# Kernel optimization log

Hardware: AMD Instinct MI355X
Metric: run time of the kernel (lower is better)

The kernel has to match this reference:

```python
import jax, jax.numpy as jnp
import numpy as np

NE = 200000   # num_entities
NR = 16       # num_relations
D  = 128      # embed_dim
B  = 4096     # batch
S  = 64       # neighbors per node
L  = 2        # num_layers
H  = 4        # attention heads (hardcoded in module)


def _ln(x, g, b, eps=1e-5):
    m = jnp.mean(x, -1, keepdims=True)
    v = jnp.mean((x - m) ** 2, -1, keepdims=True)
    return (x - m) * jax.lax.rsqrt(v + eps) * g + b


def setup_inputs() -> dict:
    key = jax.random.key(0)
    ks = jax.random.split(key, 12)
    s = 0.05
    return {
        'drug_entity_indices': jax.random.randint(ks[0], (B,), 0, NE),
        'adj_entity': jax.random.randint(ks[1], (B, S), 0, NE),
        'adj_relation': jax.random.randint(ks[2], (B, S), 0, NR),
        'edge_weights': jax.random.uniform(ks[3], (B, S), dtype=jnp.float32),
        'entity_emb': jax.random.normal(ks[4], (NE, D), jnp.float32) * s,
        'W_rgcn': jax.random.normal(ks[5], (L, NR, D, D), jnp.float32) * s,
        'res_w': jax.random.normal(ks[6], (L, D, D), jnp.float32) * s,
        'res_b': jnp.zeros((L, D), jnp.float32),
        'proj_w': jax.random.normal(ks[7], (L, D, D), jnp.float32) * s,
        'proj_b': jnp.zeros((L, D), jnp.float32),
        'ln_g': jnp.ones((L, D), jnp.float32),
        'ln_b': jnp.zeros((L, D), jnp.float32),
        'in_proj_w': jax.random.normal(ks[8], (3 * D, D), jnp.float32) * s,
        'in_proj_b': jnp.zeros((3 * D,), jnp.float32),
        'out_proj_w': jax.random.normal(ks[9], (D, D), jnp.float32) * s,
        'out_proj_b': jnp.zeros((D,), jnp.float32),
        'fln_g': jnp.ones((D,), jnp.float32),
        'fln_b': jnp.zeros((D,), jnp.float32),
    }


def reference(drug_entity_indices, adj_entity, adj_relation, edge_weights,
              entity_emb, W_rgcn, res_w, res_b, proj_w, proj_b, ln_g, ln_b,
              in_proj_w, in_proj_b, out_proj_w, out_proj_b, fln_g, fln_b):
    node = entity_emb[drug_entity_indices]           # [B,D] combined_emb
    nbr = entity_emb[adj_entity]                     # [B,S,D]
    # Route each edge to its relation: sum_s nbr*ew*[rel==r] then one GEMM per relation
    # (mathematically identical to the per-relation masked matmul loop in torch).
    onehot = jax.nn.one_hot(adj_relation, NR, dtype=node.dtype)      # [B,S,R]
    pre = jnp.einsum('bsd,bsr->brd', nbr * edge_weights[..., None], onehot)
    outs = []
    for l in range(L):
        msgs = jnp.einsum('brd,rde->be', pre, W_rgcn[l])             # [B,D]
        h = jax.nn.relu(node + msgs + node @ res_w[l].T + res_b[l])  # RGCNAggregator
        node = _ln(h @ proj_w[l].T + proj_b[l] + node, ln_g[l], ln_b[l])
        outs.append(node)
    x = jnp.stack(outs, 0)                           # [L,B,D] seq-first
    qkv = x @ in_proj_w.T + in_proj_b
    q, k, v = jnp.split(qkv, 3, axis=-1)
    hd = D // H
    def heads(t):
        return t.reshape(L, B, H, hd).transpose(1, 2, 0, 3)          # [B,H,L,hd]
    q, k, v = heads(q), heads(k), heads(v)
    att = jax.nn.softmax(jnp.einsum('bhld,bhmd->bhlm', q, k) / np.sqrt(hd).astype(np.float32), axis=-1)
    o = jnp.einsum('bhlm,bhmd->bhld', att, v).transpose(2, 0, 1, 3).reshape(L, B, D)
    o = o @ out_proj_w.T + out_proj_b
    return _ln(o.mean(0), fln_g, fln_b)              # [B,D]
```

## Files before the change

kernel.cpp:

```cpp
#include <hip/hip_runtime.h>
#include <math.h>

#define NRREL 16
#define DDIM 128
#define BBATCH 4096
#define SNBR 64

typedef __attribute__((ext_vector_type(8))) short short8;
typedef __attribute__((ext_vector_type(4))) float floatx4;

__device__ __forceinline__ unsigned short f2bf(float f) {
    unsigned u = __builtin_bit_cast(unsigned, f);
    u += 0x7fffu + ((u >> 16) & 1u);
    return (unsigned short)(u >> 16);
}
__device__ __forceinline__ float bf2f(unsigned short u) {
    return __builtin_bit_cast(float, ((unsigned)u) << 16);
}

extern "C" __global__ __launch_bounds__(256)
void k_front(const int* __restrict__ drug, const int* __restrict__ adj_e,
             const int* __restrict__ adj_r, const float* __restrict__ ew,
             const float* __restrict__ emb, const float* __restrict__ W_rgcn,
             const float* __restrict__ res_w, const float* __restrict__ proj_w,
             const float* __restrict__ in_w, const float* __restrict__ out_w,
             unsigned short* __restrict__ pre_bf, float* __restrict__ node_f,
             unsigned short* __restrict__ Wcat, unsigned short* __restrict__ resw,
             unsigned short* __restrict__ projw, unsigned short* __restrict__ inw,
             unsigned short* __restrict__ outw)
{
    __shared__ union {
        struct {
            unsigned short rows_bf[64 * 136];
            int memb[16][64];
            int cnt[16];
            int sent[64];
            float swt[64];
        } g;
        struct { float tileT[64 * 65]; } w;
    } sm;

    const int bid = blockIdx.x, t = threadIdx.x;

    if (bid < BBATCH) {
        const int b = bid;
        if (t < 16) sm.g.cnt[t] = 0;
        __syncthreads();
        if (t < 64) {
            sm.g.sent[t] = adj_e[b * SNBR + t];
            sm.g.swt[t]  = ew[b * SNBR + t];
            int r = adj_r[b * SNBR + t];
            int slot = atomicAdd(&sm.g.cnt[r], 1);
            sm.g.memb[r][slot] = t;
        }
        if (t >= 64 && t < 96) {
            int tt = t - 64;
            float4 nf = *(const float4*)(emb + (size_t)drug[b] * DDIM + 4 * tt);
            *(float4*)(node_f + (size_t)b * DDIM + 4 * tt) = nf;
        }
        __syncthreads();
        #pragma unroll
        for (int i = 0; i < 8; ++i) {
            int flat = t + 256 * i;
            int s = flat >> 5, c = flat & 31;
            float wq = sm.g.swt[s];
            float4 v = *(const float4*)(emb + (size_t)sm.g.sent[s] * DDIM + 4 * c);
            ushort4 o = { f2bf(v.x * wq), f2bf(v.y * wq), f2bf(v.z * wq), f2bf(v.w * wq) };
            *(ushort4*)(sm.g.rows_bf + s * 136 + 4 * c) = o;
        }
        __syncthreads();
        const int r = t >> 4, g8 = t & 15;
        const int n = sm.g.cnt[r];
        float acc[8] = {0.f, 0.f, 0.f, 0.f, 0.f, 0.f, 0.f, 0.f};
        for (int j = 0; j < n; ++j) {
            int s = sm.g.memb[r][j];
            short8 rv = *(const short8*)(sm.g.rows_bf + s * 136 + 8 * g8);
            #pragma unroll
            for (int jj = 0; jj < 8; ++jj) acc[jj] += bf2f((unsigned short)rv[jj]);
        }
        short8 o;
        #pragma unroll
        for (int jj = 0; jj < 8; ++jj) o[jj] = (short)f2bf(acc[jj]);
        *(short8*)(pre_bf + (size_t)b * 2048 + r * DDIM + 8 * g8) = o;
    } else if (bid < BBATCH + 128) {
        const int bid2 = bid - BBATCH;
        const int l = bid2 >> 6, rem = bid2 & 63;
        const int k0 = (rem >> 1) * 64, e0 = (rem & 1) * 64;
        #pragma unroll
        for (int i = 0; i < 4; ++i) {
            int flat = t + 256 * i;
            int k = flat >> 4, c = flat & 15;
            float4 v = *(const float4*)(W_rgcn + ((size_t)(l * 2048 + k0 + k)) * 128 + e0 + 4 * c);
            sm.w.tileT[(4 * c + 0) * 65 + k] = v.x;
            sm.w.tileT[(4 * c + 1) * 65 + k] = v.y;
            sm.w.tileT[(4 * c + 2) * 65 + k] = v.z;
            sm.w.tileT[(4 * c + 3) * 65 + k] = v.w;
        }
        __syncthreads();
        const int e = t >> 2, m = t & 3;
        #pragma unroll
        for (int half = 0; half < 2; ++half) {
            int kk = 16 * m + 8 * half;
            short8 o;
            #pragma unroll
            for (int j = 0; j < 8; ++j) o[j] = (short)f2bf(sm.w.tileT[e * 65 + kk + j]);
            *(short8*)(Wcat + ((size_t)(l * 128 + e0 + e)) * 2048 + k0 + kk) = o;
        }
    } else {
        int j4 = ((bid - BBATCH - 128) * 256 + t) * 4;
        const float* src; unsigned short* dst; int off;
        if (j4 < 32768)       { src = res_w;  dst = resw;  off = j4; }
        else if (j4 < 65536)  { src = proj_w; dst = projw; off = j4 - 32768; }
        else if (j4 < 114688) { src = in_w;   dst = inw;   off = j4 - 65536; }
        else                  { src = out_w;  dst = outw;  off = j4 - 114688; }
        float4 v = *(const float4*)(src + off);
        ushort4 o = { f2bf(v.x), f2bf(v.y), f2bf(v.z), f2bf(v.w) };
        *(ushort4*)(dst + off) = o;
    }
}

extern "C" __global__ __launch_bounds__(256)
void k_msgs(const unsigned short* __restrict__ pre_bf,
            const unsigned short* __restrict__ Wcat, float* __restrict__ part)
{
    const int wave = threadIdx.x >> 6, wm = wave >> 1, wn = wave & 1;
    const int r0 = blockIdx.x * 64 + wm * 32;
    const int c0 = blockIdx.y * 64 + wn * 32;
    const int koff = blockIdx.z * 512;
    const int lane = threadIdx.x & 63, l15 = lane & 15, q = lane >> 4;
    floatx4 acc[2][2] = {};
    const unsigned short* a0 = pre_bf + (size_t)(r0 + l15) * 2048 + koff + q * 8;
    const unsigned short* a1 = a0 + (size_t)16 * 2048;
    const unsigned short* b0 = Wcat + (size_t)(c0 + l15) * 2048 + koff + q * 8;
    const unsigned short* b1 = b0 + (size_t)16 * 2048;
    #pragma unroll 2
    for (int k = 0; k < 512; k += 32) {
        short8 A0 = *(const short8*)(a0 + k);
        short8 A1 = *(const short8*)(a1 + k);
        short8 B0 = *(const short8*)(b0 + k);
        short8 B1 = *(const short8*)(b1 + k);
        acc[0][0] = __builtin_amdgcn_mfma_f32_16x16x32_bf16(A0, B0, acc[0][0], 0, 0, 0);
        acc[0][1] = __builtin_amdgcn_mfma_f32_16x16x32_bf16(A0, B1, acc[0][1], 0, 0, 0);
        acc[1][0] = __builtin_amdgcn_mfma_f32_16x16x32_bf16(A1, B0, acc[1][0], 0, 0, 0);
        acc[1][1] = __builtin_amdgcn_mfma_f32_16x16x32_bf16(A1, B1, acc[1][1], 0, 0, 0);
    }
    float* dst = part + (size_t)blockIdx.z * BBATCH * 256;
    for (int mi = 0; mi < 2; ++mi)
        for (int ni = 0; ni < 2; ++ni) {
            int gc = c0 + ni * 16 + l15;
            #pragma unroll
            for (int r = 0; r < 4; ++r)
                dst[(size_t)(r0 + mi * 16 + 4 * q + r) * 256 + gc] = acc[mi][ni][r];
        }
}

extern "C" __global__ __launch_bounds__(256)
void k_tail(const float* __restrict__ node_fg, const float* __restrict__ part,
            const unsigned short* __restrict__ resw, const unsigned short* __restrict__ projw,
            const float* __restrict__ res_b, const float* __restrict__ proj_b,
            const float* __restrict__ ln_g, const float* __restrict__ ln_b,
            const unsigned short* __restrict__ inw, const float* __restrict__ in_b,
            const unsigned short* __restrict__ outw, const float* __restrict__ out_b,
            const float* __restrict__ fg, const float* __restrict__ fb,
            float* __restrict__ outp)
{
    __shared__ float          node_ln[16 * 132];
    __shared__ unsigned short node_b16[16 * 136];
    __shared__ unsigned short h_b16[16 * 136];
    __shared__ float          msum[16 * 260];
    __shared__ unsigned short xs_l[32 * 136];
    __shared__ unsigned short qkvl[32 * 392];
    __shared__ float          psum[4][16], psq[4][16];

    const int t = threadIdx.x, w = t >> 6, lane = t & 63, l15 = lane & 15, q = lane >> 4;
    const int r0 = blockIdx.x * 16;

    #pragma unroll
    for (int i = 0; i < 2; ++i) {
        int flat = t + 256 * i;
        int rr = flat >> 5, c = flat & 31;
        float4 v = *(const float4*)(node_fg + (size_t)(r0 + rr) * DDIM + 4 * c);
        *(float4*)(node_ln + rr * 132 + 4 * c) = v;
        ushort4 o = { f2bf(v.x), f2bf(v.y), f2bf(v.z), f2bf(v.w) };
        *(ushort4*)(node_b16 + rr * 136 + 4 * c) = o;
    }
    #pragma unroll
    for (int i = 0; i < 4; ++i) {
        int flat = t + 256 * i;
        int rr = flat >> 6, c = flat & 63;
        float4 s = {0.f, 0.f, 0.f, 0.f};
        #pragma unroll
        for (int kc = 0; kc < 4; ++kc) {
            float4 v = *(const float4*)(part + ((size_t)kc * BBATCH + r0 + rr) * 256 + 4 * c);
            s.x += v.x; s.y += v.y; s.z += v.z; s.w += v.w;
        }
        *(float4*)(msum + rr * 260 + 4 * c) = s;
    }
    __syncthreads();

    for (int l = 0; l < 2; ++l) {
        {
            const unsigned short* Bw = resw + (size_t)l * DDIM * DDIM;
            floatx4 acc[2] = {};
            const unsigned short* ap = node_b16 + l15 * 136 + 8 * q;
            #pragma unroll
            for (int kk = 0; kk < DDIM; kk += 32) {
                short8 A = *(const short8*)(ap + kk);
                #pragma unroll
                for (int ni = 0; ni < 2; ++ni) {
                    short8 B = *(const short8*)(Bw + (size_t)(32 * w + ni * 16 + l15) * DDIM + kk + 8 * q);
                    acc[ni] = __builtin_amdgcn_mfma_f32_16x16x32_bf16(A, B, acc[ni], 0, 0, 0);
                }
            }
            #pragma unroll
            for (int ni = 0; ni < 2; ++ni) {
                int gc = 32 * w + ni * 16 + l15;
                float rb = res_b[l * DDIM + gc];
                #pragma unroll
                for (int r = 0; r < 4; ++r) {
                    int lr = 4 * q + r;
                    float v = acc[ni][r] + rb + node_ln[lr * 132 + gc] + msum[lr * 260 + l * DDIM + gc];
                    h_b16[lr * 136 + gc] = f2bf(v > 0.f ? v : 0.f);
                }
            }
        }
        __syncthreads();
        {
            const unsigned short* Bw = projw + (size_t)l * DDIM * DDIM;
            floatx4 acc[2] = {};
            const unsigned short* ap = h_b16 + l15 * 136 + 8 * q;
            #pragma unroll
            for (int kk = 0; kk < DDIM; kk += 32) {
                short8 A = *(const short8*)(ap + kk);
                #pragma unroll
                for (int ni = 0; ni < 2; ++ni) {
                    short8 B = *(const short8*)(Bw + (size_t)(32 * w + ni * 16 + l15) * DDIM + kk + 8 * q);
                    acc[ni] = __builtin_amdgcn_mfma_f32_16x16x32_bf16(A, B, acc[ni], 0, 0, 0);
                }
            }
            float vv[2][4];
            float s4[4] = {0, 0, 0, 0}, sq4[4] = {0, 0, 0, 0};
            #pragma unroll
            for (int ni = 0; ni < 2; ++ni) {
                int gc = 32 * w + ni * 16 + l15;
                float pb = proj_b[l * DDIM + gc];
                #pragma unroll
                for (int r = 0; r < 4; ++r) {
                    int lr = 4 * q + r;
                    float v = acc[ni][r] + pb + node_ln[lr * 132 + gc];
                    vv[ni][r] = v; s4[r] += v; sq4[r] += v * v;
                }
            }
            #pragma unroll
            for (int r = 0; r < 4; ++r)
                #pragma unroll
                for (int off2 = 8; off2 >= 1; off2 >>= 1) {
                    s4[r] += __shfl_xor(s4[r], off2, 64);
                    sq4[r] += __shfl_xor(sq4[r], off2, 64);
                }
            if (l15 == 0) {
                #pragma unroll
                for (int r = 0; r < 4; ++r) {
                    psum[w][4 * q + r] = s4[r];
                    psq[w][4 * q + r] = sq4[r];
                }
            }
            __syncthreads();
            #pragma unroll
            for (int ni = 0; ni < 2; ++ni) {
                int gc = 32 * w + ni * 16 + l15;
                float g2 = ln_g[l * DDIM + gc], bb = ln_b[l * DDIM + gc];
                #pragma unroll
                for (int r = 0; r < 4; ++r) {
                    int lr = 4 * q + r;
                    float ssum = psum[0][lr] + psum[1][lr] + psum[2][lr] + psum[3][lr];
                    float ssq  = psq[0][lr] + psq[1][lr] + psq[2][lr] + psq[3][lr];
                    float mean = ssum * (1.f / DDIM);
                    float var = ssq * (1.f / DDIM) - mean * mean;
                    float val = (vv[ni][r] - mean) * rsqrtf(var + 1e-5f) * g2 + bb;
                    node_ln[lr * 132 + gc] = val;
                    unsigned short ub = f2bf(val);
                    node_b16[lr * 136 + gc] = ub;
                    xs_l[(2 * lr + l) * 136 + gc] = ub;
                }
            }
            __syncthreads();
        }
    }

    {
        floatx4 acc[12] = {};
        const unsigned short* ap = xs_l + (16 * (w & 1) + l15) * 136 + 8 * q;
        #pragma unroll
        for (int kk = 0; kk < DDIM; kk += 32) {
            short8 A = *(const short8*)(ap + kk);
            #pragma unroll
            for (int ni = 0; ni < 12; ++ni) {
                short8 B = *(const short8*)(inw + (size_t)(192 * (w >> 1) + ni * 16 + l15) * DDIM + kk + 8 * q);
                acc[ni] = __builtin_amdgcn_mfma_f32_16x16x32_bf16(A, B, acc[ni], 0, 0, 0);
            }
        }
        #pragma unroll
        for (int ni = 0; ni < 12; ++ni) {
            int gc = 192 * (w >> 1) + ni * 16 + l15;
            float ib = in_b[gc];
            #pragma unroll
            for (int r = 0; r < 4; ++r)
                qkvl[(16 * (w & 1) + 4 * q + r) * 392 + gc] = f2bf(acc[ni][r] + ib);
        }
    }
    __syncthreads();

    if (t < 128) {
        int g4 = t >> 3, j = t & 7;
        const unsigned short* row0 = qkvl + (2 * g4) * 392;
        const unsigned short* row1 = row0 + 392;
        float p00 = 0.f, p01 = 0.f, p10 = 0.f, p11 = 0.f;
        #pragma unroll
        for (int dd = 0; dd < 16; ++dd) {
            int d = 16 * j + dd;
            float q0 = bf2f(row0[d]), k0 = bf2f(row0[128 + d]);
            float q1 = bf2f(row1[d]), k1 = bf2f(row1[128 + d]);
            p00 = fmaf(q0, k0, p00); p01 = fmaf(q0, k1, p01);
            p10 = fmaf(q1, k0, p10); p11 = fmaf(q1, k1, p11);
        }
        p00 += __shfl_xor(p00, 1, 64); p01 += __shfl_xor(p01, 1, 64);
        p10 += __shfl_xor(p10, 1, 64); p11 += __shfl_xor(p11, 1, 64);
        const float sc = 0.17677669529663687f;
        p00 *= sc; p01 *= sc; p10 *= sc; p11 *= sc;
        float m0 = fmaxf(p00, p01), e00 = expf(p00 - m0), e01 = expf(p01 - m0);
        float i0 = 1.f / (e00 + e01);
        float m1 = fmaxf(p10, p11), e10 = expf(p10 - m1), e11 = expf(p11 - m1);
        float i1 = 1.f / (e10 + e11);
        #pragma unroll
        for (int dd = 0; dd < 16; ++dd) {
            int d = 16 * j + dd;
            float v0 = bf2f(row0[256 + d]), v1 = bf2f(row1[256 + d]);
            xs_l[(2 * g4) * 136 + d]     = f2bf((e00 * v0 + e01 * v1) * i0);
            xs_l[(2 * g4 + 1) * 136 + d] = f2bf((e10 * v0 + e11 * v1) * i1);
        }
    }
    __syncthreads();

    {
        floatx4 acc[4] = {};
        const unsigned short* ap = xs_l + (16 * (w & 1) + l15) * 136 + 8 * q;
        #pragma unroll
        for (int kk = 0; kk < DDIM; kk += 32) {
            short8 A = *(const short8*)(ap + kk);
            #pragma unroll
            for (int ni = 0; ni < 4; ++ni) {
                short8 B = *(const short8*)(outw + (size_t)(64 * (w >> 1) + ni * 16 + l15) * DDIM + kk + 8 * q);
                acc[ni] = __builtin_amdgcn_mfma_f32_16x16x32_bf16(A, B, acc[ni], 0, 0, 0);
            }
        }
        float av[4][2];
        float s2[2] = {0, 0}, sq2[2] = {0, 0};
        #pragma unroll
        for (int ni = 0; ni < 4; ++ni) {
            int gc = 64 * (w >> 1) + ni * 16 + l15;
            float ob = out_b[gc];
            #pragma unroll
            for (int rr = 0; rr < 2; ++rr) {
                float v = 0.5f * (acc[ni][2 * rr] + acc[ni][2 * rr + 1]) + ob;
                av[ni][rr] = v; s2[rr] += v; sq2[rr] += v * v;
            }
        }
        #pragma unroll
        for (int rr = 0; rr < 2; ++rr)
            #pragma unroll
            for (int off2 = 8; off2 >= 1; off2 >>= 1) {
                s2[rr] += __shfl_xor(s2[rr], off2, 64);
                sq2[rr] += __shfl_xor(sq2[rr], off2, 64);
            }
        if (l15 == 0) {
            #pragma unroll
            for (int rr = 0; rr < 2; ++rr) {
                psum[w][2 * q + rr] = s2[rr];
                psq[w][2 * q + rr] = sq2[rr];
            }
        }
        __syncthreads();
        #pragma unroll
        for (int ni = 0; ni < 4; ++ni) {
            int gc = 64 * (w >> 1) + ni * 16 + l15;
            float g2 = fg[gc], bb = fb[gc];
            #pragma unroll
            for (int rr = 0; rr < 2; ++rr) {
                int idx = 2 * q + rr;
                int bl = 8 * (w & 1) + idx;
                float ssum = psum[w & 1][idx] + psum[(w & 1) + 2][idx];
                float ssq  = psq[w & 1][idx] + psq[(w & 1) + 2][idx];
                float mean = ssum * (1.f / DDIM);
                float var = ssq * (1.f / DDIM) - mean * mean;
                outp[(size_t)(r0 + bl) * DDIM + gc] = (av[ni][rr] - mean) * rsqrtf(var + 1e-5f) * g2 + bb;
            }
        }
    }
}

extern "C" void kernel_launch(void* const* d_in, const int* in_sizes, int n_in,
                              void* d_out, int out_size, void* d_ws, size_t ws_size,
                              hipStream_t stream) {
    const int*   drug_idx = (const int*)d_in[0];
    const int*   adj_ent  = (const int*)d_in[1];
    const int*   adj_rel  = (const int*)d_in[2];
    const float* ew       = (const float*)d_in[3];
    const float* emb      = (const float*)d_in[4];
    const float* W_rgcn   = (const float*)d_in[5];
    const float* res_w    = (const float*)d_in[6];
    const float* res_b    = (const float*)d_in[7];
    const float* proj_w   = (const float*)d_in[8];
    const float* proj_b   = (const float*)d_in[9];
    const float* ln_g     = (const float*)d_in[10];
    const float* ln_b     = (const float*)d_in[11];
    const float* in_w     = (const float*)d_in[12];
    const float* in_b     = (const float*)d_in[13];
    const float* out_w    = (const float*)d_in[14];
    const float* out_b    = (const float*)d_in[15];
    const float* fg       = (const float*)d_in[16];
    const float* fb       = (const float*)d_in[17];
    float* outp = (float*)d_out;

    char* ws = (char*)d_ws;
    size_t off = 0;
    auto alloc = [&](size_t bytes) { size_t o = off; off = (off + bytes + 255) & ~(size_t)255; return o; };
    unsigned short* pre_bf  = (unsigned short*)(ws + alloc((size_t)BBATCH * 2048 * 2));
    float*          node_f  = (float*)         (ws + alloc((size_t)BBATCH * 128 * 4));
    float*          part    = (float*)         (ws + alloc((size_t)4 * BBATCH * 256 * 4));
    unsigned short* Wcat    = (unsigned short*)(ws + alloc((size_t)256 * 2048 * 2));
    unsigned short* resw    = (unsigned short*)(ws + alloc((size_t)2 * 128 * 128 * 2));
    unsigned short* projw   = (unsigned short*)(ws + alloc((size_t)2 * 128 * 128 * 2));
    unsigned short* inw     = (unsigned short*)(ws + alloc((size_t)384 * 128 * 2));
    unsigned short* outw    = (unsigned short*)(ws + alloc((size_t)128 * 128 * 2));

    hipLaunchKernelGGL(k_front, dim3(BBATCH + 256), dim3(256), 0, stream,
                       drug_idx, adj_ent, adj_rel, ew, emb, W_rgcn,
                       res_w, proj_w, in_w, out_w,
                       pre_bf, node_f, Wcat, resw, projw, inw, outw);
    hipLaunchKernelGGL(k_msgs, dim3(64, 4, 4), dim3(256), 0, stream, pre_bf, Wcat, part);
    hipLaunchKernelGGL(k_tail, dim3(256), dim3(256), 0, stream,
                       node_f, part, resw, projw, res_b, proj_b, ln_g, ln_b,
                       inw, in_b, outw, out_b, fg, fb, outp);
}
```

Before: 246.0 us.

## Fuse message GEMM into tail kernel and gather neighbors directly in front kernel

Removes the separate split-K message GEMM kernel and its fp32 partial-sum buffer. The tail kernel now computes each 16-row block's full K=2048 product against Wcat directly into shared memory. The front kernel also stops staging weighted neighbor rows in LDS as bf16 and instead accumulates fp32 FMAs straight from global embedding rows per relation. In exchange, the tail GEMM runs with only 256 blocks over a long K loop, so parallelism drops. Each neighbor row is now read from global memory by 16-thread groups instead of being staged once.

After: 241.4 us. Within noise of the previous version (-1.9%).

```diff
diff --git a/kernel.cpp b/kernel.cpp
--- a/kernel.cpp
+++ b/kernel.cpp
@@ -31,7 +31,6 @@
 {
     __shared__ union {
         struct {
-            unsigned short rows_bf[64 * 136];
             int memb[16][64];
             int cnt[16];
             int sent[64];
@@ -59,24 +58,19 @@
             *(float4*)(node_f + (size_t)b * DDIM + 4 * tt) = nf;
         }
         __syncthreads();
-        #pragma unroll
-        for (int i = 0; i < 8; ++i) {
-            int flat = t + 256 * i;
-            int s = flat >> 5, c = flat & 31;
-            float wq = sm.g.swt[s];
-            float4 v = *(const float4*)(emb + (size_t)sm.g.sent[s] * DDIM + 4 * c);
-            ushort4 o = { f2bf(v.x * wq), f2bf(v.y * wq), f2bf(v.z * wq), f2bf(v.w * wq) };
-            *(ushort4*)(sm.g.rows_bf + s * 136 + 4 * c) = o;
-        }
-        __syncthreads();
         const int r = t >> 4, g8 = t & 15;
         const int n = sm.g.cnt[r];
         float acc[8] = {0.f, 0.f, 0.f, 0.f, 0.f, 0.f, 0.f, 0.f};
         for (int j = 0; j < n; ++j) {
             int s = sm.g.memb[r][j];
-            short8 rv = *(const short8*)(sm.g.rows_bf + s * 136 + 8 * g8);
-            #pragma unroll
-            for (int jj = 0; jj < 8; ++jj) acc[jj] += bf2f((unsigned short)rv[jj]);
+            float wq = sm.g.swt[s];
+            const float* p = emb + (size_t)sm.g.sent[s] * DDIM + 8 * g8;
+            float4 v0 = *(const float4*)p;
+            float4 v1 = *(const float4*)(p + 4);
+            acc[0] = fmaf(v0.x, wq, acc[0]); acc[1] = fmaf(v0.y, wq, acc[1]);
+            acc[2] = fmaf(v0.z, wq, acc[2]); acc[3] = fmaf(v0.w, wq, acc[3]);
+            acc[4] = fmaf(v1.x, wq, acc[4]); acc[5] = fmaf(v1.y, wq, acc[5]);
+            acc[6] = fmaf(v1.z, wq, acc[6]); acc[7] = fmaf(v1.w, wq, acc[7]);
         }
         short8 o;
         #pragma unroll
@@ -120,42 +114,8 @@
 }
 
 extern "C" __global__ __launch_bounds__(256)
-void k_msgs(const unsigned short* __restrict__ pre_bf,
-            const unsigned short* __restrict__ Wcat, float* __restrict__ part)
-{
-    const int wave = threadIdx.x >> 6, wm = wave >> 1, wn = wave & 1;
-    const int r0 = blockIdx.x * 64 + wm * 32;
-    const int c0 = blockIdx.y * 64 + wn * 32;
-    const int koff = blockIdx.z * 512;
-    const int lane = threadIdx.x & 63, l15 = lane & 15, q = lane >> 4;
-    floatx4 acc[2][2] = {};
-    const unsigned short* a0 = pre_bf + (size_t)(r0 + l15) * 2048 + koff + q * 8;
-    const unsigned short* a1 = a0 + (size_t)16 * 2048;
-    const unsigned short* b0 = Wcat + (size_t)(c0 + l15) * 2048 + koff + q * 8;
-    const unsigned short* b1 = b0 + (size_t)16 * 2048;
-    #pragma unroll 2
-    for (int k = 0; k < 512; k += 32) {
-        short8 A0 = *(const short8*)(a0 + k);
-        short8 A1 = *(const short8*)(a1 + k);
-        short8 B0 = *(const short8*)(b0 + k);
-        short8 B1 = *(const short8*)(b1 + k);
-        acc[0][0] = __builtin_amdgcn_mfma_f32_16x16x32_bf16(A0, B0, acc[0][0], 0, 0, 0);
-        acc[0][1] = __builtin_amdgcn_mfma_f32_16x16x32_bf16(A0, B1, acc[0][1], 0, 0, 0);
-        acc[1][0] = __builtin_amdgcn_mfma_f32_16x16x32_bf16(A1, B0, acc[1][0], 0, 0, 0);
-        acc[1][1] = __builtin_amdgcn_mfma_f32_16x16x32_bf16(A1, B1, acc[1][1], 0, 0, 0);
-    }
-    float* dst = part + (size_t)blockIdx.z * BBATCH * 256;
-    for (int mi = 0; mi < 2; ++mi)
-        for (int ni = 0; ni < 2; ++ni) {
-            int gc = c0 + ni * 16 + l15;
-            #pragma unroll
-            for (int r = 0; r < 4; ++r)
-                dst[(size_t)(r0 + mi * 16 + 4 * q + r) * 256 + gc] = acc[mi][ni][r];
-        }
-}
-
-extern "C" __global__ __launch_bounds__(256)
-void k_tail(const float* __restrict__ node_fg, const float* __restrict__ part,
+void k_tail(const unsigned short* __restrict__ pre_bf, const unsigned short* __restrict__ Wcat,
+            const float* __restrict__ node_fg,
             const unsigned short* __restrict__ resw, const unsigned short* __restrict__ projw,
             const float* __restrict__ res_b, const float* __restrict__ proj_b,
             const float* __restrict__ ln_g, const float* __restrict__ ln_b,
@@ -184,17 +144,27 @@
         ushort4 o = { f2bf(v.x), f2bf(v.y), f2bf(v.z), f2bf(v.w) };
         *(ushort4*)(node_b16 + rr * 136 + 4 * c) = o;
     }
-    #pragma unroll
-    for (int i = 0; i < 4; ++i) {
-        int flat = t + 256 * i;
-        int rr = flat >> 6, c = flat & 63;
-        float4 s = {0.f, 0.f, 0.f, 0.f};
-        #pragma unroll
-        for (int kc = 0; kc < 4; ++kc) {
-            float4 v = *(const float4*)(part + ((size_t)kc * BBATCH + r0 + rr) * 256 + 4 * c);
-            s.x += v.x; s.y += v.y; s.z += v.z; s.w += v.w;
-        }
-        *(float4*)(msum + rr * 260 + 4 * c) = s;
+
+    {
+        floatx4 macc[4] = {};
+        const unsigned short* ap = pre_bf + (size_t)(r0 + l15) * 2048 + 8 * q;
+        const unsigned short* bp = Wcat + (size_t)(64 * w + l15) * 2048 + 8 * q;
+        #pragma unroll 2
+        for (int k = 0; k < 2048; k += 32) {
+            short8 A = *(const short8*)(ap + k);
+            #pragma unroll
+            for (int ni = 0; ni < 4; ++ni) {
+                short8 B = *(const short8*)(bp + (size_t)(ni * 16) * 2048 + k);
+                macc[ni] = __builtin_amdgcn_mfma_f32_16x16x32_bf16(A, B, macc[ni], 0, 0, 0);
+            }
+        }
+        #pragma unroll
+        for (int ni = 0; ni < 4; ++ni) {
+            int gc = 64 * w + ni * 16 + l15;
+            #pragma unroll
+            for (int r = 0; r < 4; ++r)
+                msum[(4 * q + r) * 260 + gc] = macc[ni][r];
+        }
     }
     __syncthreads();
 
@@ -427,7 +397,6 @@
     auto alloc = [&](size_t bytes) { size_t o = off; off = (off + bytes + 255) & ~(size_t)255; return o; };
     unsigned short* pre_bf  = (unsigned short*)(ws + alloc((size_t)BBATCH * 2048 * 2));
     float*          node_f  = (float*)         (ws + alloc((size_t)BBATCH * 128 * 4));
-    float*          part    = (float*)         (ws + alloc((size_t)4 * BBATCH * 256 * 4));
     unsigned short* Wcat    = (unsigned short*)(ws + alloc((size_t)256 * 2048 * 2));
     unsigned short* resw    = (unsigned short*)(ws + alloc((size_t)2 * 128 * 128 * 2));
     unsigned short* projw   = (unsigned short*)(ws + alloc((size_t)2 * 128 * 128 * 2));
@@ -438,8 +407,7 @@
                        drug_idx, adj_ent, adj_rel, ew, emb, W_rgcn,
                        res_w, proj_w, in_w, out_w,
                        pre_bf, node_f, Wcat, resw, projw, inw, outw);
-    hipLaunchKernelGGL(k_msgs, dim3(64, 4, 4), dim3(256), 0, stream, pre_bf, Wcat, part);
     hipLaunchKernelGGL(k_tail, dim3(256), dim3(256), 0, stream,
-                       node_f, part, resw, projw, res_b, proj_b, ln_g, ln_b,
+                       pre_bf, Wcat, node_f, resw, projw, res_b, proj_b, ln_g, ln_b,
                        inw, in_b, outw, out_b, fg, fb, outp);
 }
```
